# Kernel tuning notes

Measured on AMD Instinct MI355X. Metric: run time of the kernel, lower is better.

Reference implementation:

```python
import jax, jax.numpy as jnp
import numpy as np

Y0 = 0.28209479177387814  # Y_0^0 spherical harmonic (degree-0 basis)
CUTOFF = 4.6
K_COUL = 0.529
ENERGY_STD = 1.0
HEADS = 8
N, E, C, L, MID = 32768, 524288, 16, 4, 32
KC = C // 2  # channels_div = 2 -> key/value channels


def _radial(ef, W1, b1, W2, b2, W3, b3):
    # radial profile MLP producing per-edge conv weights
    h = jax.nn.relu(ef @ W1 + b1)
    h = jax.nn.relu(h @ W2 + b2)
    return h @ W3 + b3


def _conv_msg(x_src, ef, bscale, W1, b1, W2, b2, W3, b3, c_out, c_in):
    # degree-0 tensor-field conv: per-edge weight matrix times source feats, times basis
    R = _radial(ef, W1, b1, W2, b2, W3, b3).reshape(-1, c_out, c_in)
    return jnp.einsum('eoi,ei->eo', R, x_src) * bscale[:, None]


def _forward(species, src, dst, rel_pos, emb, kv_W1, kv_b1, kv_W2, kv_b2, kv_W3, kv_b3, Wq, Wproj, fin_W1, fin_b1, fin_W2, fin_b2, fin_W3, fin_b3, Wself, mlp_W1, mlp_b1, mlp_W2, mlp_b2, mlp_W3, mlp_b3):
    n = species.shape[0]
    dist = jnp.linalg.norm(rel_pos, axis=1)
    xc = dist / CUTOFF
    in_cut = dist < CUTOFF
    x2 = jnp.minimum(jnp.where(in_cut, xc * xc, 0.0), 1.0 - 1e-6)
    scale = jnp.where(in_cut, jnp.exp(3.0 - 3.0 / (1.0 - x2)), 0.0)  # bump_fn k=3
    bscale = Y0 * scale  # basis scaled by cutoff envelope per edge
    semb = emb[species - 1]          # [N,C]
    x = semb                         # degree-0 node feats
    # edge feats: (C-1) zero radial-basis channels + distance
    ef = jnp.concatenate([jnp.zeros((dist.shape[0], C - 1), dist.dtype), dist[:, None]], axis=1)
    dh = KC // HEADS
    for l in range(kv_W1.shape[0]):
        kv = _conv_msg(x[src], ef, bscale, kv_W1[l], kv_b1[l], kv_W2[l], kv_b2[l], kv_W3[l], kv_b3[l], 2 * KC, C)
        val, key_ = kv[:, :KC], kv[:, KC:]
        q = x @ Wq[l].T              # [N,KC]
        logits = jnp.einsum('ehd,ehd->eh', key_.reshape(-1, HEADS, dh), q[dst].reshape(-1, HEADS, dh)) / np.sqrt(dh)
        mx = jax.ops.segment_max(logits, dst, num_segments=n)
        w = scale[:, None] * jnp.exp(logits - mx[dst])   # weighted edge softmax
        denom = jax.ops.segment_sum(w, dst, num_segments=n)
        attn = w / jnp.maximum(denom[dst], 1e-20)
        z = (attn[:, :, None] * val.reshape(-1, HEADS, dh)).reshape(-1, KC)
        agg = jax.ops.segment_sum(z, dst, num_segments=n)
        x = jnp.concatenate([agg, x], axis=1) @ Wproj[l].T  # project(cat(attn_out, skip))
        ef = ef + x[src]             # edge feature update via copy_u
    m = _conv_msg(x[src], ef, bscale, fin_W1, fin_b1, fin_W2, fin_b2, fin_W3, fin_b3, C, C)
    feats = jax.ops.segment_sum(m, dst, num_segments=n) + x @ Wself.T  # pooled conv + self-interaction
    cat = jnp.concatenate([semb, feats], axis=1)
    h = jax.nn.silu(cat @ mlp_W1 + mlp_b1)
    h = jax.nn.silu(h @ mlp_W2 + mlp_b2)
    learned = (h @ mlp_W3 + mlp_b3)[:, 0]
    Z = species.astype(dist.dtype)
    Zu, Zv = Z[src], Z[dst]
    raw = K_COUL * Zu * Zv / (2.0 * dist)
    au = 0.8854 * 0.529 / (Zu ** 0.23 + Zv ** 0.23)
    xx = dist / au
    screen = (0.1818 * jnp.exp(-3.2 * xx) + 0.5099 * jnp.exp(-0.9423 * xx)
              + 0.2802 * jnp.exp(-0.4028 * xx) + 0.02817 * jnp.exp(-0.2016 * xx))
    coul = jax.ops.segment_sum(raw * screen * scale, dst, num_segments=n) / ENERGY_STD
    atom_e = (learned + coul) * ENERGY_STD
    return jnp.sum(atom_e)  # SumPooling over a single graph, forces=False


def setup_inputs() -> dict:
    key = jax.random.key(0)
    ks = jax.random.split(key, 32)
    species = jax.random.randint(ks[0], (N,), 1, 90, dtype=jnp.int32)
    src = jax.random.randint(ks[1], (E,), 0, N, dtype=jnp.int32)
    dst = jax.random.randint(ks[2], (E,), 0, N, dtype=jnp.int32)
    d = jax.random.normal(ks[3], (E, 3))
    d = d / jnp.linalg.norm(d, axis=1, keepdims=True)
    r = jax.random.uniform(ks[4], (E, 1), minval=0.5, maxval=5.5)
    rel_pos = (d * r).astype(jnp.float32)
    g = lambda k, sh, fan: (jax.random.normal(k, sh) / np.sqrt(fan)).astype(jnp.float32)
    return dict(
        species=species, src=src, dst=dst, rel_pos=rel_pos,
        emb=g(ks[5], (100, C), 1),
        kv_W1=g(ks[6], (L, C, MID), C), kv_b1=jnp.zeros((L, MID), jnp.float32),
        kv_W2=g(ks[7], (L, MID, MID), MID), kv_b2=jnp.zeros((L, MID), jnp.float32),
        kv_W3=g(ks[8], (L, MID, 2 * KC * C), MID), kv_b3=jnp.zeros((L, 2 * KC * C), jnp.float32),
        Wq=g(ks[9], (L, KC, C), C),
        Wproj=g(ks[10], (L, C, KC + C), KC + C),
        fin_W1=g(ks[11], (C, MID), C), fin_b1=jnp.zeros((MID,), jnp.float32),
        fin_W2=g(ks[12], (MID, MID), MID), fin_b2=jnp.zeros((MID,), jnp.float32),
        fin_W3=g(ks[13], (MID, C * C), MID), fin_b3=jnp.zeros((C * C,), jnp.float32),
        Wself=g(ks[14], (C, C), C),
        mlp_W1=g(ks[15], (2 * C, C), 2 * C), mlp_b1=jnp.zeros((C,), jnp.float32),
        mlp_W2=g(ks[16], (C, C), C), mlp_b2=jnp.zeros((C,), jnp.float32),
        mlp_W3=g(ks[17], (C, 1), C), mlp_b3=jnp.zeros((1,), jnp.float32),
    )


def reference(species, src, dst, rel_pos, emb, kv_W1, kv_b1, kv_W2, kv_b2, kv_W3, kv_b3, Wq, Wproj, fin_W1, fin_b1, fin_W2, fin_b2, fin_W3, fin_b3, Wself, mlp_W1, mlp_b1, mlp_W2, mlp_b2, mlp_W3, mlp_b3):
    return _forward(species, src, dst, rel_pos, emb, kv_W1, kv_b1, kv_W2, kv_b2, kv_W3, kv_b3, Wq, Wproj, fin_W1, fin_b1, fin_W2, fin_b2, fin_W3, fin_b3, Wself, mlp_W1, mlp_b1, mlp_W2, mlp_b2, mlp_W3, mlp_b3)
```

## Files before the change

### kernel.cpp

```cpp
#include <hip/hip_runtime.h>

constexpr float F_Y0     = 0.28209479177387814f;
constexpr float F_CUTOFF = 4.6f;

typedef short short8 __attribute__((ext_vector_type(8)));
typedef float f32x4  __attribute__((ext_vector_type(4)));
typedef float float2v __attribute__((ext_vector_type(2)));

__device__ __forceinline__ float siluf(float v) { return v / (1.0f + __expf(-v)); }

__device__ __forceinline__ unsigned pk2(float a, float b) {
  unsigned r;
  asm("v_cvt_pk_bf16_f32 %0, %1, %2" : "=v"(r) : "v"(a), "v"(b));
  return r;
}
__device__ __forceinline__ float xbf(unsigned d, int h) {
  return __uint_as_float(h ? (d & 0xffff0000u) : (d << 16));
}
__device__ __forceinline__ float2v pkmul2(float2v a, float2v b) {
  float2v d;
  asm("v_pk_mul_f32 %0, %1, %2" : "=v"(d) : "v"(a), "v"(b));
  return d;
}

union FragU { uint4 u; short8 s; };

__device__ __forceinline__ void load16(const float* p, float* r) {
  const float4* p4 = (const float4*)p;
#pragma unroll
  for (int i = 0; i < 4; i++) {
    float4 t = p4[i];
    r[4*i] = t.x; r[4*i+1] = t.y; r[4*i+2] = t.z; r[4*i+3] = t.w;
  }
}
__device__ __forceinline__ void store16(float* p, const float* r) {
  float4* p4 = (float4*)p;
#pragma unroll
  for (int i = 0; i < 4; i++) p4[i] = make_float4(r[4*i], r[4*i+1], r[4*i+2], r[4*i+3]);
}

__device__ __forceinline__ void block_reduce_store(float v, float* part) {
  __shared__ float sred[4];
  int tid = threadIdx.x;
#pragma unroll
  for (int off = 32; off > 0; off >>= 1) v += __shfl_down(v, off, 64);
  if ((tid & 63) == 0) sred[tid >> 6] = v;
  __syncthreads();
  if (tid == 0) part[blockIdx.x] = sred[0] + sred[1] + sred[2] + sred[3];
}

__global__ __launch_bounds__(256) void k_pre(
    const int* __restrict__ species, const int* __restrict__ src, const int* __restrict__ dst,
    const float* __restrict__ rel_pos,
    float* __restrict__ dist_, float* __restrict__ scale_,
    int* __restrict__ cnt,
    float* __restrict__ coul_part,
    int* __restrict__ srcP, float* __restrict__ distP, float* __restrict__ scaleP, int E)
{
  __shared__ float zpow[128];
  int tid = threadIdx.x;
  if (tid < 128) zpow[tid] = __powf((float)tid, 0.23f);
  __syncthreads();

  int e = blockIdx.x * 256 + tid;
  float ce = 0.0f;
  if (e < E) {
    float px = rel_pos[3*(size_t)e + 0];
    float py = rel_pos[3*(size_t)e + 1];
    float pz = rel_pos[3*(size_t)e + 2];
    float dist = sqrtf(px*px + py*py + pz*pz);
    float xc = dist * (1.0f / F_CUTOFF);
    bool in_cut = dist < F_CUTOFF;
    float x2 = in_cut ? xc * xc : 0.0f;
    x2 = fminf(x2, 1.0f - 1e-6f);
    float sc = in_cut ? __expf(3.0f - 3.0f / (1.0f - x2)) : 0.0f;
    dist_[e] = dist;
    scale_[e] = sc;
    srcP[e]   = 0;
    distP[e]  = 1.0f;
    scaleP[e] = 0.0f;
    if (sc > 0.0f) {
      atomicAdd(&cnt[dst[e]], 1);
      int spu = species[src[e]], spv = species[dst[e]];
      float Zu = (float)spu;
      float Zv = (float)spv;
      float raw = 0.529f * Zu * Zv / (2.0f * dist);
      float au = 0.8854f * 0.529f / (zpow[spu] + zpow[spv]);
      float xx = dist / au;
      float screen = 0.1818f   * __expf(-3.2f    * xx)
                   + 0.5099f   * __expf(-0.9423f * xx)
                   + 0.2802f   * __expf(-0.4028f * xx)
                   + 0.02817f  * __expf(-0.2016f * xx);
      ce = raw * screen * sc;
    }
  }
  block_reduce_store(ce, coul_part);
}

__global__ __launch_bounds__(256) void k_scan1(
    const int* __restrict__ cnt, int* __restrict__ row_ptr, int* __restrict__ bsum)
{
  __shared__ int s[256];
  int tid = threadIdx.x;
  int n = blockIdx.x * 256 + tid;
  int v = cnt[n];
  s[tid] = v;
  __syncthreads();
#pragma unroll
  for (int off = 1; off < 256; off <<= 1) {
    int t = (tid >= off) ? s[tid - off] : 0;
    __syncthreads();
    s[tid] += t;
    __syncthreads();
  }
  row_ptr[n] = s[tid] - v;
  if (tid == 255) bsum[blockIdx.x] = s[255];
}

__global__ __launch_bounds__(128) void k_scan2(int* __restrict__ bsum, int* __restrict__ boff)
{
  __shared__ int s[128];
  int tid = threadIdx.x;
  int v = bsum[tid];
  s[tid] = v;
  __syncthreads();
#pragma unroll
  for (int off = 1; off < 128; off <<= 1) {
    int t = (tid >= off) ? s[tid - off] : 0;
    __syncthreads();
    s[tid] += t;
    __syncthreads();
  }
  boff[tid] = s[tid] - v;
}

__global__ __launch_bounds__(256) void k_scan3(
    int* __restrict__ row_ptr, int* __restrict__ row_cur,
    const int* __restrict__ boff, const int* __restrict__ cnt, int N)
{
  int n = blockIdx.x * 256 + threadIdx.x;
  int rp = row_ptr[n] + boff[blockIdx.x];
  row_ptr[n] = rp;
  row_cur[n] = rp;
  if (n == N - 1) row_ptr[N] = rp + cnt[n];
}

__global__ __launch_bounds__(256) void k_scatter_perm(
    const int* __restrict__ dst, const float* __restrict__ scale_,
    int* __restrict__ row_cur,
    int* __restrict__ perm, int E)
{
  int e = blockIdx.x * 256 + threadIdx.x;
  if (e >= E) return;
  if (scale_[e] > 0.0f) {
    int pos = atomicAdd(&row_cur[dst[e]], 1);
    perm[pos] = e;
  }
}

__global__ __launch_bounds__(256) void k_permute(
    const int* __restrict__ perm,
    const int* __restrict__ src, const float* __restrict__ dist_, const float* __restrict__ scale_,
    int* __restrict__ srcP, float* __restrict__ distP, float* __restrict__ scaleP,
    const int* __restrict__ eactp)
{
  int i = blockIdx.x * 256 + threadIdx.x;
  if (i >= eactp[0]) return;
  int e = perm[i];
  srcP[i]   = src[e];
  distP[i]  = dist_[e];
  scaleP[i] = scale_[e];
}

__global__ __launch_bounds__(256) void k_prepack(
    const float* __restrict__ kv_W3, const float* __restrict__ kv_b3,
    const float* __restrict__ fin_W3, const float* __restrict__ fin_b3,
    const float* __restrict__ kv_W2, const float* __restrict__ fin_W2,
    const float* __restrict__ kv_W1, const float* __restrict__ fin_W1,
    uint4* __restrict__ WF)
{
  int t = blockIdx.x * 256 + threadIdx.x;
  if (t >= 5 * 21 * 64) return;
  int lyr = t / (21 * 64);
  int rem = t - lyr * 21 * 64;
  int f = rem >> 6;
  int l = rem & 63;
  int qq = l >> 4;
  int o = l & 15;
  const float* W3 = (lyr < 4) ? (kv_W3 + (size_t)lyr * 32 * 256) : fin_W3;
  const float* B3 = (lyr < 4) ? (kv_b3 + (size_t)lyr * 256) : fin_b3;
  const float* W2 = (lyr < 4) ? (kv_W2 + (size_t)lyr * 32 * 32) : fin_W2;
  const float* W1 = (lyr < 4) ? (kv_W1 + (size_t)lyr * 16 * 32) : fin_W1;
  float v[8];
#pragma unroll
  for (int j = 0; j < 8; j++) {
    if (f < 16) {
      int kk = f * 32 + qq * 8 + j;
      int m = kk >> 4, i = kk & 15;
      v[j] = W3[m * 256 + o * 16 + i];
    } else if (f == 16) {
      int r = qq * 8 + j;
      int mp = r >> 4, i = r & 15;
      v[j] = mp ? 0.0f : B3[o * 16 + i];
    } else if (f < 19) {
      int c = f - 17;
      int p = qq * 8 + j;
      int m = (p & 1) ? (16 + (p >> 1)) : (p >> 1);
      v[j] = W2[m * 32 + c * 16 + o];
    } else {
      int c = f - 19;
      int k = qq * 8 + j;
      v[j] = (k < 16) ? W1[k * 32 + c * 16 + o] : 0.0f;
    }
  }
  uint4 dw;
  dw.x = pk2(v[0], v[1]);
  dw.y = pk2(v[2], v[3]);
  dw.z = pk2(v[4], v[5]);
  dw.w = pk2(v[6], v[7]);
  WF[t] = dw;
}

__global__ __launch_bounds__(256) void k_node_init(
    const int* __restrict__ species, const float* __restrict__ emb,
    const float* __restrict__ Wq0,
    float* __restrict__ x, float* __restrict__ q, int N)
{
  int n = blockIdx.x * 256 + threadIdx.x;
  if (n >= N) return;
  int sp = species[n] - 1;
  float xv[16];
  load16(emb + (size_t)sp * 16, xv);
  store16(x + (size_t)n * 16, xv);
  float qv[8];
#pragma unroll
  for (int h = 0; h < 8; h++) {
    float a = 0.f;
#pragma unroll
    for (int i = 0; i < 16; i++) a += Wq0[h * 16 + i] * xv[i];
    qv[h] = a;
  }
  float4* qp = (float4*)(q + (size_t)n * 8);
  qp[0] = make_float4(qv[0], qv[1], qv[2], qv[3]);
  qp[1] = make_float4(qv[4], qv[5], qv[6], qv[7]);
}

template <int MODE>
__global__ __launch_bounds__(256, 7) void k_edge_conv(
    const int* __restrict__ srcP,
    const float* __restrict__ scaleP, const float* __restrict__ distP,
    const float* __restrict__ xsum, const float* __restrict__ x,
    const float* __restrict__ W1, const float* __restrict__ B1,
    const float* __restrict__ B2,
    const uint4* __restrict__ WF,
    unsigned* __restrict__ kvB, const int* __restrict__ eactp)
{
  if (blockIdx.x * 64 >= eactp[0]) return;
  __shared__ unsigned smem[4 * 1344];
  int tid = threadIdx.x;
  int w = __builtin_amdgcn_readfirstlane(tid >> 6);
  int l = tid & 63;
  int quad = l >> 4;
  int lo = l & 15;
  unsigned* WS  = smem + w * 1344;
  float*    xsS = (float*)WS;
  unsigned* xsB = WS + 320;
  unsigned* efB = WS + 512;
  unsigned* h1P = WS + 704;
  unsigned* h2P = WS + 1024;

  int ebw = blockIdx.x * 64 + w * 16;

  float b2a = B2[lo], b2b = B2[16 + lo];
  float scv[4];
#pragma unroll
  for (int r = 0; r < 4; r++) scv[r] = scaleP[ebw + quad * 4 + r];

  {
    int e4 = l >> 2, c4 = l & 3;
    int s4 = srcP[ebw + e4];
    float4 xv4 = ((const float4*)(x + (size_t)s4 * 16))[c4];
    float4 ev4;
    if (MODE == 2) {
      ev4 = ((const float4*)(xsum + (size_t)s4 * 16))[c4];
      if (c4 == 3) ev4.w += distP[ebw + e4];
    }
    *(float4*)&xsS[e4 * 20 + c4 * 4] = xv4;
    uint2 xp; xp.x = pk2(xv4.x, xv4.y); xp.y = pk2(xv4.z, xv4.w);
    *(uint2*)&xsB[e4 * 12 + c4 * 2] = xp;
    if (MODE == 2) {
      uint2 ep; ep.x = pk2(ev4.x, ev4.y); ep.y = pk2(ev4.z, ev4.w);
      *(uint2*)&efB[e4 * 12 + c4 * 2] = ep;
    }
  }

  if (MODE == 0) {
    float dd = distP[ebw + lo];
#pragma unroll
    for (int jj = 0; jj < 4; jj++) {
      int d = quad * 4 + jj;
      float v0 = fmaxf(B1[d]      + dd * W1[15 * 32 + d],      0.f);
      float v1 = fmaxf(B1[d + 16] + dd * W1[15 * 32 + d + 16], 0.f);
      h1P[lo * 20 + d] = pk2(v0, v1);
    }
  } else {
    float b1a = B1[lo], b1b = B1[16 + lo];
    FragU a, b0, b1;
    uint4 r = *(const uint4*)&efB[lo * 12 + (quad & 1) * 4];
    uint4 z = make_uint4(0, 0, 0, 0);
    a.u = (quad >= 2) ? z : r;
    b0.u = WF[19 * 64 + l];
    b1.u = WF[20 * 64 + l];
    f32x4 c0 = {0.f, 0.f, 0.f, 0.f};
    f32x4 c1 = {0.f, 0.f, 0.f, 0.f};
    c0 = __builtin_amdgcn_mfma_f32_16x16x32_bf16(a.s, b0.s, c0, 0, 0, 0);
    c1 = __builtin_amdgcn_mfma_f32_16x16x32_bf16(a.s, b1.s, c1, 0, 0, 0);
#pragma unroll
    for (int r2 = 0; r2 < 4; r2++)
      h1P[(quad * 4 + r2) * 20 + lo] =
          pk2(fmaxf(c0[r2] + b1a, 0.f), fmaxf(c1[r2] + b1b, 0.f));
  }

  {
    FragU a, b0, b1;
    a.u = *(const uint4*)&h1P[lo * 20 + quad * 4];
    b0.u = WF[17 * 64 + l];
    b1.u = WF[18 * 64 + l];
    f32x4 hc0 = {0.f, 0.f, 0.f, 0.f};
    f32x4 hc1 = {0.f, 0.f, 0.f, 0.f};
    hc0 = __builtin_amdgcn_mfma_f32_16x16x32_bf16(a.s, b0.s, hc0, 0, 0, 0);
    hc1 = __builtin_amdgcn_mfma_f32_16x16x32_bf16(a.s, b1.s, hc1, 0, 0, 0);
    int pp = (lo & 1) * 8 + (lo >> 1);
    float b2av = b2a, b2bv = b2b;
#pragma unroll
    for (int r = 0; r < 4; r++)
      h2P[(quad * 4 + r) * 20 + pp] =
          pk2(fmaxf(hc0[r] + b2av, 0.f), fmaxf(hc1[r] + b2bv, 0.f));
  }

  float2v xs2[4];
  {
    const float4* xr = (const float4*)&xsS[lo * 20 + (quad & 1) * 8];
#pragma unroll
    for (int i = 0; i < 2; i++) {
      float4 t = xr[i];
      float2v a; a.x = t.x; a.y = t.y;
      float2v b; b.x = t.z; b.y = t.w;
      xs2[2 * i]     = a;
      xs2[2 * i + 1] = b;
    }
  }
  uint4 hq0 = *(const uint4*)&h2P[lo * 20 + (quad >> 1) * 8];
  uint4 hq1 = *(const uint4*)&h2P[lo * 20 + (quad >> 1) * 8 + 4];
  unsigned hdw[8] = {hq0.x, hq0.y, hq0.z, hq0.w, hq1.x, hq1.y, hq1.z, hq1.w};

  f32x4 acc = {0.f, 0.f, 0.f, 0.f};
  {
    FragU a, b;
    uint4 r = *(const uint4*)&xsB[lo * 12 + (quad & 1) * 4];
    uint4 z = make_uint4(0, 0, 0, 0);
    a.u = (quad >= 2) ? z : r;
    b.u = WF[16 * 64 + l];
    acc = __builtin_amdgcn_mfma_f32_16x16x32_bf16(a.s, b.s, acc, 0, 0, 0);
  }

#pragma unroll
  for (int f = 0; f < 16; f++) {
    float hm = xbf(hdw[f & 7], f >> 3);
    float2v hm2; hm2.x = hm; hm2.y = hm;
    float2v p0 = pkmul2(hm2, xs2[0]);
    float2v p1 = pkmul2(hm2, xs2[1]);
    float2v p2 = pkmul2(hm2, xs2[2]);
    float2v p3 = pkmul2(hm2, xs2[3]);
    FragU a, b;
    a.u.x = pk2(p0.x, p0.y);
    a.u.y = pk2(p1.x, p1.y);
    a.u.z = pk2(p2.x, p2.y);
    a.u.w = pk2(p3.x, p3.y);
    b.u = WF[f * 64 + l];
    acc = __builtin_amdgcn_mfma_f32_16x16x32_bf16(a.s, b.s, acc, 0, 0, 0);
  }

#pragma unroll
  for (int r = 0; r < 4; r++) {
    int e = quad * 4 + r;
    ((float*)h2P)[e * 20 + lo] = acc[r] * (F_Y0 * scv[r]);
  }
  {
    int e2 = l >> 2, c = l & 3;
    const float* row = (const float*)&h2P[e2 * 20 + c * 4];
    float4 t = *(const float4*)row;
    uint2 pkd;
    pkd.x = pk2(t.x, t.y);
    pkd.y = pk2(t.z, t.w);
    *(uint2*)(kvB + ((size_t)(ebw + e2) * 8 + c * 2)) = pkd;
  }
}

template <bool INIT>
__global__ __launch_bounds__(256) void k_agg_update(
    const int* __restrict__ row_ptr, const float* __restrict__ scaleP,
    const unsigned* __restrict__ kvB, const float* __restrict__ qin,
    const float* __restrict__ xin,
    const float* __restrict__ Wproj, const float* __restrict__ Wq_next,
    float* __restrict__ xout, float* __restrict__ qout, float* __restrict__ xsum, int N)
{
  __shared__ float sA[16 * 8];
  __shared__ float sX[16 * 17];
  __shared__ float sN[16 * 17];
  int tid = threadIdx.x;
  int nl = tid >> 4;
  int t16 = tid & 15;
  int h = t16 & 7;
  int p = t16 >> 3;
  int n = blockIdx.x * 16 + nl;
  int hd = h >> 1, hh = h & 1;

  float qh = qin[(size_t)n * 8 + h];
  int j0 = row_ptr[n], j1 = row_ptr[n + 1];
  float num = 0.f, den = 0.f;
  int j = j0 + p;
  for (; j + 6 < j1; j += 8) {
    unsigned va = kvB[(size_t)j * 8 + hd];
    unsigned ka = kvB[(size_t)j * 8 + 4 + hd];
    unsigned vb = kvB[(size_t)(j + 2) * 8 + hd];
    unsigned kb = kvB[(size_t)(j + 2) * 8 + 4 + hd];
    unsigned vc = kvB[(size_t)(j + 4) * 8 + hd];
    unsigned kc = kvB[(size_t)(j + 4) * 8 + 4 + hd];
    unsigned vd = kvB[(size_t)(j + 6) * 8 + hd];
    unsigned kd = kvB[(size_t)(j + 6) * 8 + 4 + hd];
    float sa = scaleP[j];
    float sb = scaleP[j + 2];
    float sc = scaleP[j + 4];
    float sd = scaleP[j + 6];
    float wa = sa * __expf(fminf(xbf(ka, hh) * qh, 60.0f));
    float wb = sb * __expf(fminf(xbf(kb, hh) * qh, 60.0f));
    float wc = sc * __expf(fminf(xbf(kc, hh) * qh, 60.0f));
    float wd = sd * __expf(fminf(xbf(kd, hh) * qh, 60.0f));
    num += wa * xbf(va, hh) + wb * xbf(vb, hh) + wc * xbf(vc, hh) + wd * xbf(vd, hh);
    den += (wa + wb) + (wc + wd);
  }
  for (; j < j1; j += 2) {
    float val = xbf(kvB[(size_t)j * 8 + hd], hh);
    float key = xbf(kvB[(size_t)j * 8 + 4 + hd], hh);
    float lg = fminf(key * qh, 60.0f);
    float wv = scaleP[j] * __expf(lg);
    num += wv * val;
    den += wv;
  }
  num += __shfl_xor(num, 8, 64);
  den += __shfl_xor(den, 8, 64);
  if (p == 0) sA[nl * 8 + h] = num / fmaxf(den, 1e-20f);
  sX[nl * 17 + t16] = xin[(size_t)n * 16 + t16];
  __syncthreads();

  float cat[24];
#pragma unroll
  for (int jj = 0; jj < 8; jj++) cat[jj] = sA[nl * 8 + jj];
#pragma unroll
  for (int jj = 0; jj < 16; jj++) cat[8 + jj] = sX[nl * 17 + jj];
  float xn = 0.f;
#pragma unroll
  for (int jj = 0; jj < 24; jj++) xn += Wproj[t16 * 24 + jj] * cat[jj];
  xout[(size_t)n * 16 + t16] = xn;
  if (INIT) {
    xsum[(size_t)n * 16 + t16] = xn;
  } else {
    xsum[(size_t)n * 16 + t16] += xn;
  }
  sN[nl * 17 + t16] = xn;
  __syncthreads();

  if (p == 0) {
    float a = 0.f;
#pragma unroll
    for (int i = 0; i < 16; i++) a += Wq_next[h * 16 + i] * sN[nl * 17 + i];
    qout[(size_t)n * 8 + h] = a;
  }
}

__global__ __launch_bounds__(256) void k_feats_final(
    const int* __restrict__ row_ptr, const unsigned* __restrict__ kvB,
    const float* __restrict__ x,
    const int* __restrict__ species, const float* __restrict__ emb,
    const float* __restrict__ Wself,
    const float* __restrict__ mW1, const float* __restrict__ mb1,
    const float* __restrict__ mW2, const float* __restrict__ mb2,
    const float* __restrict__ mW3, const float* __restrict__ mb3,
    float* __restrict__ learn_part, int N)
{
  __shared__ float sX[16 * 20];
  __shared__ float sC[16 * 40];
  __shared__ float sH[16 * 20];
  int tid = threadIdx.x;
  int nl = tid >> 4;
  int o = tid & 15;
  int n = blockIdx.x * 16 + nl;
  int od = o >> 1, oh = o & 1;

  int j0 = row_ptr[n], j1 = row_ptr[n + 1];
  float ft = 0.f;
  int j = j0;
  for (; j + 3 < j1; j += 4) {
    unsigned a = kvB[(size_t)j * 8 + od];
    unsigned b = kvB[(size_t)(j + 1) * 8 + od];
    unsigned c = kvB[(size_t)(j + 2) * 8 + od];
    unsigned d = kvB[(size_t)(j + 3) * 8 + od];
    ft += (xbf(a, oh) + xbf(b, oh)) + (xbf(c, oh) + xbf(d, oh));
  }
  for (; j < j1; ++j) ft += xbf(kvB[(size_t)j * 8 + od], oh);

  if (o < 4) {
    float4 v = ((const float4*)(x + (size_t)n * 16))[o];
    *(float4*)&sX[nl * 20 + o * 4] = v;
  } else if (o < 8) {
    int sp = species[n] - 1;
    float4 v = ((const float4*)(emb + (size_t)sp * 16))[o - 4];
    *(float4*)&sC[nl * 40 + (o - 4) * 4] = v;
  }
  __syncthreads();

  float xv[16];
  load16(&sX[nl * 20], xv);
  float a = ft;
#pragma unroll
  for (int i = 0; i < 16; i++) a += Wself[o * 16 + i] * xv[i];
  sC[nl * 40 + 16 + o] = a;
  __syncthreads();

  float cat[32];
  load16(&sC[nl * 40], cat);
  load16(&sC[nl * 40 + 16], cat + 16);
  float hh = mb1[o];
#pragma unroll
  for (int k = 0; k < 32; k++) hh += cat[k] * mW1[k * 16 + o];
  hh = siluf(hh);
  sH[nl * 20 + o] = hh;
  __syncthreads();

  float hv[16];
  load16(&sH[nl * 20], hv);
  float h2 = mb2[o];
#pragma unroll
  for (int k = 0; k < 16; k++) h2 += hv[k] * mW2[k * 16 + o];
  h2 = siluf(h2);
  float contrib = h2 * mW3[o] + ((o == 0) ? mb3[0] : 0.f);
  block_reduce_store(contrib, learn_part);
}

__global__ __launch_bounds__(256) void k_finalize(
    const float* __restrict__ coul_part, int nc,
    const float* __restrict__ learn_part, int nl,
    float* __restrict__ out)
{
  __shared__ float sred[4];
  int tid = threadIdx.x;
  float v = 0.f;
  for (int i = tid; i < nc; i += 256) v += coul_part[i];
  for (int i = tid; i < nl; i += 256) v += learn_part[i];
#pragma unroll
  for (int off = 32; off > 0; off >>= 1) v += __shfl_down(v, off, 64);
  if ((tid & 63) == 0) sred[tid >> 6] = v;
  __syncthreads();
  if (tid == 0) out[0] = sred[0] + sred[1] + sred[2] + sred[3];
}

extern "C" void kernel_launch(void* const* d_in, const int* in_sizes, int n_in,
                              void* d_out, int out_size, void* d_ws, size_t ws_size,
                              hipStream_t stream)
{
  const int*   species = (const int*)d_in[0];
  const int*   src     = (const int*)d_in[1];
  const int*   dst     = (const int*)d_in[2];
  const float* rel_pos = (const float*)d_in[3];
  const float* emb     = (const float*)d_in[4];
  const float* kv_W1   = (const float*)d_in[5];
  const float* kv_b1   = (const float*)d_in[6];
  const float* kv_W2   = (const float*)d_in[7];
  const float* kv_b2   = (const float*)d_in[8];
  const float* kv_W3   = (const float*)d_in[9];
  const float* kv_b3   = (const float*)d_in[10];
  const float* Wq      = (const float*)d_in[11];
  const float* Wproj   = (const float*)d_in[12];
  const float* fin_W1  = (const float*)d_in[13];
  const float* fin_b1  = (const float*)d_in[14];
  const float* fin_W2  = (const float*)d_in[15];
  const float* fin_b2  = (const float*)d_in[16];
  const float* fin_W3  = (const float*)d_in[17];
  const float* fin_b3  = (const float*)d_in[18];
  const float* Wself   = (const float*)d_in[19];
  const float* mlp_W1  = (const float*)d_in[20];
  const float* mlp_b1  = (const float*)d_in[21];
  const float* mlp_W2  = (const float*)d_in[22];
  const float* mlp_b2  = (const float*)d_in[23];
  const float* mlp_W3  = (const float*)d_in[24];
  const float* mlp_b3  = (const float*)d_in[25];

  const int N = in_sizes[0];
  const int E = in_sizes[1];
  const int nblk_e = (E + 255) / 256;
  const int nblk_n = (N + 255) / 256;
  const int nblk_f = N / 16;

  char* p = (char*)d_ws;
  auto alloc = [&](size_t bytes) -> void* {
    void* r = (void*)p;
    p += (bytes + 255) & ~(size_t)255;
    return r;
  };
  float*    dist_   = (float*)alloc((size_t)E * 4);
  float*    scale_  = (float*)alloc((size_t)E * 4);
  float*    distP   = (float*)alloc((size_t)E * 4);
  float*    scaleP  = (float*)alloc((size_t)E * 4);
  int*      srcP    = (int*)  alloc((size_t)E * 4);
  int*      perm    = (int*)  alloc((size_t)E * 4);
  unsigned* kvB     = (unsigned*)alloc((size_t)E * 8 * 4);
  float*    xA      = (float*)alloc((size_t)N * 16 * 4);
  float*    xB      = (float*)alloc((size_t)N * 16 * 4);
  float*    xsum    = (float*)alloc((size_t)N * 16 * 4);
  float*    q       = (float*)alloc((size_t)N * 8 * 4);
  int*      cnt     = (int*)  alloc((size_t)N * 4);
  int*      row_ptr = (int*)  alloc((size_t)(N + 1) * 4);
  int*      row_cur = (int*)  alloc((size_t)N * 4);
  int*      bsum    = (int*)  alloc(128 * 4);
  int*      boff    = (int*)  alloc(128 * 4);
  uint4*    WF      = (uint4*)alloc((size_t)5 * 21 * 64 * 16);
  float*    coul_part  = (float*)alloc((size_t)nblk_e * 4);
  float*    learn_part = (float*)alloc((size_t)nblk_f * 4);

  const int* eactp = row_ptr + N;

  dim3 blk(256);
  dim3 egrid(nblk_e);
  dim3 cgrid(E / 64);
  dim3 ngrid(nblk_n);
  dim3 augrid(N / 16);
  dim3 fgrid(nblk_f);

  hipMemsetAsync(cnt, 0, (size_t)N * 4, stream);

  k_prepack<<<dim3(27), blk, 0, stream>>>(kv_W3, kv_b3, fin_W3, fin_b3,
                                          kv_W2, fin_W2, kv_W1, fin_W1, WF);

  k_pre<<<egrid, blk, 0, stream>>>(species, src, dst, rel_pos, dist_, scale_,
                                   cnt, coul_part, srcP, distP, scaleP, E);
  k_scan1<<<ngrid, blk, 0, stream>>>(cnt, row_ptr, bsum);
  k_scan2<<<dim3(1), dim3(128), 0, stream>>>(bsum, boff);
  k_scan3<<<ngrid, blk, 0, stream>>>(row_ptr, row_cur, boff, cnt, N);
  k_scatter_perm<<<egrid, blk, 0, stream>>>(dst, scale_, row_cur, perm, E);
  k_permute<<<egrid, blk, 0, stream>>>(perm, src, dist_, scale_,
                                       srcP, distP, scaleP, eactp);

  k_node_init<<<ngrid, blk, 0, stream>>>(species, emb, Wq, xA, q, N);

  float* xin = xA;
  float* xout = xB;
  for (int l = 0; l < 4; l++) {
    const float* W1 = kv_W1 + (size_t)l * 16 * 32;
    const float* B1 = kv_b1 + (size_t)l * 32;
    const float* B2 = kv_b2 + (size_t)l * 32;
    const uint4* WFl = WF + (size_t)l * 21 * 64;
    const float* Wqn = Wq + (size_t)((l < 3) ? (l + 1) : 0) * 8 * 16;
    if (l == 0) {
      k_edge_conv<0><<<cgrid, blk, 0, stream>>>(srcP, scaleP, distP, xsum, xin,
                                                W1, B1, B2, WFl, kvB, eactp);
    } else {
      k_edge_conv<2><<<cgrid, blk, 0, stream>>>(srcP, scaleP, distP, xsum, xin,
                                                W1, B1, B2, WFl, kvB, eactp);
    }
    if (l == 0) {
      k_agg_update<true><<<augrid, blk, 0, stream>>>(row_ptr, scaleP, kvB, q, xin,
                                                     Wproj, Wqn, xout, q, xsum, N);
    } else {
      k_agg_update<false><<<augrid, blk, 0, stream>>>(row_ptr, scaleP, kvB, q, xin,
                                                      Wproj + (size_t)l * 16 * 24, Wqn,
                                                      xout, q, xsum, N);
    }
    float* tmp = xin; xin = xout; xout = tmp;
  }

  k_edge_conv<2><<<cgrid, blk, 0, stream>>>(srcP, scaleP, distP, xsum, xin,
                                            fin_W1, fin_b1, fin_b2,
                                            WF + (size_t)4 * 21 * 64, kvB, eactp);
  k_feats_final<<<fgrid, blk, 0, stream>>>(row_ptr, kvB, xin, species, emb, Wself,
                                           mlp_W1, mlp_b1, mlp_W2, mlp_b2, mlp_W3, mlp_b3,
                                           learn_part, N);
  k_finalize<<<dim3(1), blk, 0, stream>>>(coul_part, nblk_e, learn_part, nblk_f,
                                          (float*)d_out);
}
```

Before: 361.0 us.

## Merge setup kernels, fold scan pass, widen per-node aggregation, drop intra-wave barriers

Node init and weight prepacking now run as extra blocks of the edge preprocessing kernel, and the middle scan pass is folded into the final scan pass, so several kernel launches are removed. The aggregation kernel now gives each node 32 threads instead of 16, with 8 nodes per block, and spreads edges over 4 lanes. It also drops the block barriers because each node's threads sit in one wavefront. The final MLP kernel likewise drops its __syncthreads. This relies on wavefront-lockstep LDS visibility without explicit barriers, and every scan3 block now redundantly rescans the 128 block sums.

```diff
diff --git a/kernel.cpp b/kernel.cpp
--- a/kernel.cpp
+++ b/kernel.cpp
@@ -55,14 +55,88 @@
     float* __restrict__ dist_, float* __restrict__ scale_,
     int* __restrict__ cnt,
     float* __restrict__ coul_part,
-    int* __restrict__ srcP, float* __restrict__ distP, float* __restrict__ scaleP, int E)
-{
+    int* __restrict__ srcP, float* __restrict__ distP, float* __restrict__ scaleP,
+    int E, int nblk_e, int nblk_n,
+    const float* __restrict__ emb, const float* __restrict__ Wq0,
+    float* __restrict__ x, float* __restrict__ q, int N,
+    const float* __restrict__ kv_W3, const float* __restrict__ kv_b3,
+    const float* __restrict__ fin_W3, const float* __restrict__ fin_b3,
+    const float* __restrict__ kv_W2, const float* __restrict__ fin_W2,
+    const float* __restrict__ kv_W1, const float* __restrict__ fin_W1,
+    uint4* __restrict__ WF)
+{
+  int b = blockIdx.x;
+  int tid = threadIdx.x;
+
+  if (b >= nblk_e) {
+    if (b < nblk_e + nblk_n) {
+      int n = (b - nblk_e) * 256 + tid;
+      if (n >= N) return;
+      int sp = species[n] - 1;
+      float xv[16];
+      load16(emb + (size_t)sp * 16, xv);
+      store16(x + (size_t)n * 16, xv);
+      float qv[8];
+#pragma unroll
+      for (int h = 0; h < 8; h++) {
+        float a = 0.f;
+#pragma unroll
+        for (int i = 0; i < 16; i++) a += Wq0[h * 16 + i] * xv[i];
+        qv[h] = a;
+      }
+      float4* qp = (float4*)(q + (size_t)n * 8);
+      qp[0] = make_float4(qv[0], qv[1], qv[2], qv[3]);
+      qp[1] = make_float4(qv[4], qv[5], qv[6], qv[7]);
+    } else {
+      int t = (b - nblk_e - nblk_n) * 256 + tid;
+      if (t >= 5 * 21 * 64) return;
+      int lyr = t / (21 * 64);
+      int rem = t - lyr * 21 * 64;
+      int f = rem >> 6;
+      int l = rem & 63;
+      int qq = l >> 4;
+      int o = l & 15;
+      const float* W3 = (lyr < 4) ? (kv_W3 + (size_t)lyr * 32 * 256) : fin_W3;
+      const float* B3 = (lyr < 4) ? (kv_b3 + (size_t)lyr * 256) : fin_b3;
+      const float* W2 = (lyr < 4) ? (kv_W2 + (size_t)lyr * 32 * 32) : fin_W2;
+      const float* W1 = (lyr < 4) ? (kv_W1 + (size_t)lyr * 16 * 32) : fin_W1;
+      float v[8];
+#pragma unroll
+      for (int j = 0; j < 8; j++) {
+        if (f < 16) {
+          int kk = f * 32 + qq * 8 + j;
+          int m = kk >> 4, i = kk & 15;
+          v[j] = W3[m * 256 + o * 16 + i];
+        } else if (f == 16) {
+          int r = qq * 8 + j;
+          int mp = r >> 4, i = r & 15;
+          v[j] = mp ? 0.0f : B3[o * 16 + i];
+        } else if (f < 19) {
+          int c = f - 17;
+          int p = qq * 8 + j;
+          int m = (p & 1) ? (16 + (p >> 1)) : (p >> 1);
+          v[j] = W2[m * 32 + c * 16 + o];
+        } else {
+          int c = f - 19;
+          int k = qq * 8 + j;
+          v[j] = (k < 16) ? W1[k * 32 + c * 16 + o] : 0.0f;
+        }
+      }
+      uint4 dw;
+      dw.x = pk2(v[0], v[1]);
+      dw.y = pk2(v[2], v[3]);
+      dw.z = pk2(v[4], v[5]);
+      dw.w = pk2(v[6], v[7]);
+      WF[t] = dw;
+    }
+    return;
+  }
+
   __shared__ float zpow[128];
-  int tid = threadIdx.x;
   if (tid < 128) zpow[tid] = __powf((float)tid, 0.23f);
   __syncthreads();
 
-  int e = blockIdx.x * 256 + tid;
+  int e = b * 256 + tid;
   float ce = 0.0f;
   if (e < E) {
     float px = rel_pos[3*(size_t)e + 0];
@@ -117,29 +191,26 @@
   if (tid == 255) bsum[blockIdx.x] = s[255];
 }
 
-__global__ __launch_bounds__(128) void k_scan2(int* __restrict__ bsum, int* __restrict__ boff)
-{
-  __shared__ int s[128];
-  int tid = threadIdx.x;
-  int v = bsum[tid];
-  s[tid] = v;
-  __syncthreads();
-#pragma unroll
-  for (int off = 1; off < 128; off <<= 1) {
-    int t = (tid >= off) ? s[tid - off] : 0;
-    __syncthreads();
-    s[tid] += t;
-    __syncthreads();
-  }
-  boff[tid] = s[tid] - v;
-}
-
 __global__ __launch_bounds__(256) void k_scan3(
     int* __restrict__ row_ptr, int* __restrict__ row_cur,
-    const int* __restrict__ boff, const int* __restrict__ cnt, int N)
-{
-  int n = blockIdx.x * 256 + threadIdx.x;
-  int rp = row_ptr[n] + boff[blockIdx.x];
+    const int* __restrict__ bsum, const int* __restrict__ cnt, int N)
+{
+  __shared__ int sb[128];
+  __shared__ int boffv;
+  int tid = threadIdx.x;
+  if (tid < 128) sb[tid] = bsum[tid];
+  __syncthreads();
+#pragma unroll
+  for (int off = 1; off < 128; off <<= 1) {
+    int t = (tid < 128 && tid >= off) ? sb[tid - off] : 0;
+    __syncthreads();
+    if (tid < 128) sb[tid] += t;
+    __syncthreads();
+  }
+  if (tid == 0) boffv = (blockIdx.x == 0) ? 0 : sb[blockIdx.x - 1];
+  __syncthreads();
+  int n = blockIdx.x * 256 + tid;
+  int rp = row_ptr[n] + boffv;
   row_ptr[n] = rp;
   row_cur[n] = rp;
   if (n == N - 1) row_ptr[N] = rp + cnt[n];
@@ -170,79 +241,6 @@
   srcP[i]   = src[e];
   distP[i]  = dist_[e];
   scaleP[i] = scale_[e];
-}
-
-__global__ __launch_bounds__(256) void k_prepack(
-    const float* __restrict__ kv_W3, const float* __restrict__ kv_b3,
-    const float* __restrict__ fin_W3, const float* __restrict__ fin_b3,
-    const float* __restrict__ kv_W2, const float* __restrict__ fin_W2,
-    const float* __restrict__ kv_W1, const float* __restrict__ fin_W1,
-    uint4* __restrict__ WF)
-{
-  int t = blockIdx.x * 256 + threadIdx.x;
-  if (t >= 5 * 21 * 64) return;
-  int lyr = t / (21 * 64);
-  int rem = t - lyr * 21 * 64;
-  int f = rem >> 6;
-  int l = rem & 63;
-  int qq = l >> 4;
-  int o = l & 15;
-  const float* W3 = (lyr < 4) ? (kv_W3 + (size_t)lyr * 32 * 256) : fin_W3;
-  const float* B3 = (lyr < 4) ? (kv_b3 + (size_t)lyr * 256) : fin_b3;
-  const float* W2 = (lyr < 4) ? (kv_W2 + (size_t)lyr * 32 * 32) : fin_W2;
-  const float* W1 = (lyr < 4) ? (kv_W1 + (size_t)lyr * 16 * 32) : fin_W1;
-  float v[8];
-#pragma unroll
-  for (int j = 0; j < 8; j++) {
-    if (f < 16) {
-      int kk = f * 32 + qq * 8 + j;
-      int m = kk >> 4, i = kk & 15;
-      v[j] = W3[m * 256 + o * 16 + i];
-    } else if (f == 16) {
-      int r = qq * 8 + j;
-      int mp = r >> 4, i = r & 15;
-      v[j] = mp ? 0.0f : B3[o * 16 + i];
-    } else if (f < 19) {
-      int c = f - 17;
-      int p = qq * 8 + j;
-      int m = (p & 1) ? (16 + (p >> 1)) : (p >> 1);
-      v[j] = W2[m * 32 + c * 16 + o];
-    } else {
-      int c = f - 19;
-      int k = qq * 8 + j;
-      v[j] = (k < 16) ? W1[k * 32 + c * 16 + o] : 0.0f;
-    }
-  }
-  uint4 dw;
-  dw.x = pk2(v[0], v[1]);
-  dw.y = pk2(v[2], v[3]);
-  dw.z = pk2(v[4], v[5]);
-  dw.w = pk2(v[6], v[7]);
-  WF[t] = dw;
-}
-
-__global__ __launch_bounds__(256) void k_node_init(
-    const int* __restrict__ species, const float* __restrict__ emb,
-    const float* __restrict__ Wq0,
-    float* __restrict__ x, float* __restrict__ q, int N)
-{
-  int n = blockIdx.x * 256 + threadIdx.x;
-  if (n >= N) return;
-  int sp = species[n] - 1;
-  float xv[16];
-  load16(emb + (size_t)sp * 16, xv);
-  store16(x + (size_t)n * 16, xv);
-  float qv[8];
-#pragma unroll
-  for (int h = 0; h < 8; h++) {
-    float a = 0.f;
-#pragma unroll
-    for (int i = 0; i < 16; i++) a += Wq0[h * 16 + i] * xv[i];
-    qv[h] = a;
-  }
-  float4* qp = (float4*)(q + (size_t)n * 8);
-  qp[0] = make_float4(qv[0], qv[1], qv[2], qv[3]);
-  qp[1] = make_float4(qv[4], qv[5], qv[6], qv[7]);
 }
 
 template <int MODE>
@@ -405,76 +403,67 @@
     const float* __restrict__ Wproj, const float* __restrict__ Wq_next,
     float* __restrict__ xout, float* __restrict__ qout, float* __restrict__ xsum, int N)
 {
-  __shared__ float sA[16 * 8];
-  __shared__ float sX[16 * 17];
-  __shared__ float sN[16 * 17];
-  int tid = threadIdx.x;
-  int nl = tid >> 4;
-  int t16 = tid & 15;
-  int h = t16 & 7;
-  int p = t16 >> 3;
-  int n = blockIdx.x * 16 + nl;
+  __shared__ float sA[8 * 8];
+  __shared__ float sX[8 * 16];
+  __shared__ float sN[8 * 16];
+  int tid = threadIdx.x;
+  int nl = tid >> 5;
+  int t32 = tid & 31;
+  int h = t32 & 7;
+  int p = t32 >> 3;
+  int n = blockIdx.x * 8 + nl;
   int hd = h >> 1, hh = h & 1;
+
+  if (t32 < 16) sX[nl * 16 + t32] = xin[(size_t)n * 16 + t32];
 
   float qh = qin[(size_t)n * 8 + h];
   int j0 = row_ptr[n], j1 = row_ptr[n + 1];
   float num = 0.f, den = 0.f;
   int j = j0 + p;
-  for (; j + 6 < j1; j += 8) {
+  for (; j + 4 < j1; j += 8) {
     unsigned va = kvB[(size_t)j * 8 + hd];
     unsigned ka = kvB[(size_t)j * 8 + 4 + hd];
-    unsigned vb = kvB[(size_t)(j + 2) * 8 + hd];
-    unsigned kb = kvB[(size_t)(j + 2) * 8 + 4 + hd];
-    unsigned vc = kvB[(size_t)(j + 4) * 8 + hd];
-    unsigned kc = kvB[(size_t)(j + 4) * 8 + 4 + hd];
-    unsigned vd = kvB[(size_t)(j + 6) * 8 + hd];
-    unsigned kd = kvB[(size_t)(j + 6) * 8 + 4 + hd];
+    unsigned vb = kvB[(size_t)(j + 4) * 8 + hd];
+    unsigned kb = kvB[(size_t)(j + 4) * 8 + 4 + hd];
     float sa = scaleP[j];
-    float sb = scaleP[j + 2];
-    float sc = scaleP[j + 4];
-    float sd = scaleP[j + 6];
+    float sb = scaleP[j + 4];
     float wa = sa * __expf(fminf(xbf(ka, hh) * qh, 60.0f));
     float wb = sb * __expf(fminf(xbf(kb, hh) * qh, 60.0f));
-    float wc = sc * __expf(fminf(xbf(kc, hh) * qh, 60.0f));
-    float wd = sd * __expf(fminf(xbf(kd, hh) * qh, 60.0f));
-    num += wa * xbf(va, hh) + wb * xbf(vb, hh) + wc * xbf(vc, hh) + wd * xbf(vd, hh);
-    den += (wa + wb) + (wc + wd);
-  }
-  for (; j < j1; j += 2) {
+    num += wa * xbf(va, hh) + wb * xbf(vb, hh);
+    den += wa + wb;
+  }
+  for (; j < j1; j += 4) {
     float val = xbf(kvB[(size_t)j * 8 + hd], hh);
     float key = xbf(kvB[(size_t)j * 8 + 4 + hd], hh);
-    float lg = fminf(key * qh, 60.0f);
-    float wv = scaleP[j] * __expf(lg);
+    float wv = scaleP[j] * __expf(fminf(key * qh, 60.0f));
     num += wv * val;
     den += wv;
   }
-  num += __shfl_xor(num, 8, 64);
-  den += __shfl_xor(den, 8, 64);
+  num += __shfl_xor(num, 8, 64);  den += __shfl_xor(den, 8, 64);
+  num += __shfl_xor(num, 16, 64); den += __shfl_xor(den, 16, 64);
   if (p == 0) sA[nl * 8 + h] = num / fmaxf(den, 1e-20f);
-  sX[nl * 17 + t16] = xin[(size_t)n * 16 + t16];
-  __syncthreads();
-
-  float cat[24];
-#pragma unroll
-  for (int jj = 0; jj < 8; jj++) cat[jj] = sA[nl * 8 + jj];
-#pragma unroll
-  for (int jj = 0; jj < 16; jj++) cat[8 + jj] = sX[nl * 17 + jj];
-  float xn = 0.f;
-#pragma unroll
-  for (int jj = 0; jj < 24; jj++) xn += Wproj[t16 * 24 + jj] * cat[jj];
-  xout[(size_t)n * 16 + t16] = xn;
-  if (INIT) {
-    xsum[(size_t)n * 16 + t16] = xn;
-  } else {
-    xsum[(size_t)n * 16 + t16] += xn;
-  }
-  sN[nl * 17 + t16] = xn;
-  __syncthreads();
-
-  if (p == 0) {
+
+  if (t32 < 16) {
+    float cat[24];
+#pragma unroll
+    for (int jj = 0; jj < 8; jj++) cat[jj] = sA[nl * 8 + jj];
+#pragma unroll
+    for (int jj = 0; jj < 16; jj++) cat[8 + jj] = sX[nl * 16 + jj];
+    float xn = 0.f;
+#pragma unroll
+    for (int jj = 0; jj < 24; jj++) xn += Wproj[t32 * 24 + jj] * cat[jj];
+    xout[(size_t)n * 16 + t32] = xn;
+    if (INIT) {
+      xsum[(size_t)n * 16 + t32] = xn;
+    } else {
+      xsum[(size_t)n * 16 + t32] += xn;
+    }
+    sN[nl * 16 + t32] = xn;
+  }
+  if (t32 < 8) {
     float a = 0.f;
 #pragma unroll
-    for (int i = 0; i < 16; i++) a += Wq_next[h * 16 + i] * sN[nl * 17 + i];
+    for (int i = 0; i < 16; i++) a += Wq_next[h * 16 + i] * sN[nl * 16 + i];
     qout[(size_t)n * 8 + h] = a;
   }
 }
@@ -518,7 +507,6 @@
     float4 v = ((const float4*)(emb + (size_t)sp * 16))[o - 4];
     *(float4*)&sC[nl * 40 + (o - 4) * 4] = v;
   }
-  __syncthreads();
 
   float xv[16];
   load16(&sX[nl * 20], xv);
@@ -526,17 +514,15 @@
 #pragma unroll
   for (int i = 0; i < 16; i++) a += Wself[o * 16 + i] * xv[i];
   sC[nl * 40 + 16 + o] = a;
-  __syncthreads();
 
   float cat[32];
   load16(&sC[nl * 40], cat);
   load16(&sC[nl * 40 + 16], cat + 16);
-  float hh = mb1[o];
-#pragma unroll
-  for (int k = 0; k < 32; k++) hh += cat[k] * mW1[k * 16 + o];
-  hh = siluf(hh);
-  sH[nl * 20 + o] = hh;
-  __syncthreads();
+  float hh2 = mb1[o];
+#pragma unroll
+  for (int k = 0; k < 32; k++) hh2 += cat[k] * mW1[k * 16 + o];
+  hh2 = siluf(hh2);
+  sH[nl * 20 + o] = hh2;
 
   float hv[16];
   load16(&sH[nl * 20], hv);
@@ -623,7 +609,6 @@
   int*      row_ptr = (int*)  alloc((size_t)(N + 1) * 4);
   int*      row_cur = (int*)  alloc((size_t)N * 4);
   int*      bsum    = (int*)  alloc(128 * 4);
-  int*      boff    = (int*)  alloc(128 * 4);
   uint4*    WF      = (uint4*)alloc((size_t)5 * 21 * 64 * 16);
   float*    coul_part  = (float*)alloc((size_t)nblk_e * 4);
   float*    learn_part = (float*)alloc((size_t)nblk_f * 4);
@@ -634,24 +619,23 @@
   dim3 egrid(nblk_e);
   dim3 cgrid(E / 64);
   dim3 ngrid(nblk_n);
-  dim3 augrid(N / 16);
+  dim3 augrid(N / 8);
   dim3 fgrid(nblk_f);
+  const int nblk_w = 27;
 
   hipMemsetAsync(cnt, 0, (size_t)N * 4, stream);
 
-  k_prepack<<<dim3(27), blk, 0, stream>>>(kv_W3, kv_b3, fin_W3, fin_b3,
-                                          kv_W2, fin_W2, kv_W1, fin_W1, WF);
-
-  k_pre<<<egrid, blk, 0, stream>>>(species, src, dst, rel_pos, dist_, scale_,
-                                   cnt, coul_part, srcP, distP, scaleP, E);
+  k_pre<<<dim3(nblk_e + nblk_n + nblk_w), blk, 0, stream>>>(
+      species, src, dst, rel_pos, dist_, scale_, cnt, coul_part,
+      srcP, distP, scaleP, E, nblk_e, nblk_n,
+      emb, Wq, xA, q, N,
+      kv_W3, kv_b3, fin_W3, fin_b3, kv_W2, fin_W2, kv_W1, fin_W1, WF);
+
   k_scan1<<<ngrid, blk, 0, stream>>>(cnt, row_ptr, bsum);
-  k_scan2<<<dim3(1), dim3(128), 0, stream>>>(bsum, boff);
-  k_scan3<<<ngrid, blk, 0, stream>>>(row_ptr, row_cur, boff, cnt, N);
+  k_scan3<<<ngrid, blk, 0, stream>>>(row_ptr, row_cur, bsum, cnt, N);
   k_scatter_perm<<<egrid, blk, 0, stream>>>(dst, scale_, row_cur, perm, E);
   k_permute<<<egrid, blk, 0, stream>>>(perm, src, dist_, scale_,
                                        srcP, distP, scaleP, eactp);
-
-  k_node_init<<<ngrid, blk, 0, stream>>>(species, emb, Wq, xA, q, N);
 
   float* xin = xA;
   float* xout = xB;
```

New measurement: 361.7 us. Within noise of the previous version (+0.2%).
